# Performance work log

Measured on AMD Instinct MI355X. Metric: run time of the kernel, lower is better.

## Reference

```python
import jax, jax.numpy as jnp
import numpy as np

K = 1024
D = 256
BETA = 0.25


def setup_inputs() -> dict:
    key = jax.random.key(0)
    kx, kc = jax.random.split(key)
    x = jax.random.normal(kx, (64, 32, 32, D), dtype=jnp.float32)
    limit = 1.0 / K
    codebook = jax.random.uniform(kc, (K, D), dtype=jnp.float32, minval=-limit, maxval=limit)
    return {"x": x, "codebook": codebook}


def reference(x, codebook):
    flat = x.reshape(-1, D)                                   # [N, D]
    x2 = jnp.sum(jnp.square(flat), axis=1, keepdims=True)     # [N, 1]
    e2 = jnp.sum(jnp.square(codebook), axis=1)                # [K]
    sim = flat @ codebook.T                                   # [N, K]
    dist = x2 + e2 - 2.0 * sim                                # [N, K]
    idx = jnp.argmin(dist, axis=1)                            # [N]
    q = codebook[idx].reshape(x.shape)                        # [..., D]

    q_st = jax.lax.stop_gradient(q)
    x_st = jax.lax.stop_gradient(x)
    commit = jnp.mean(jnp.square(q_st - x))
    codebk = jnp.mean(jnp.square(q - x_st))
    loss = BETA * commit + codebk

    # code-usage statistics via histogram (equivalent to mean of one-hot)
    counts = jnp.zeros((K,), dtype=x.dtype).at[idx].add(1.0)
    probs = counts / flat.shape[0]
    eps = jnp.asarray(1e-10, dtype=x.dtype)
    H = -jnp.sum(probs * jnp.log2(probs + eps))               # bits/index
    perplexity = jnp.exp(H * jnp.log(jnp.asarray(2.0, dtype=x.dtype)))
    usage = jnp.sum((probs > 0).astype(x.dtype)) / float(K)

    y = x + jax.lax.stop_gradient(q - x)                      # straight-through
    return y, idx, loss, perplexity, usage, H
```

## Files before the change

### kernel.cpp

```cpp
#include <hip/hip_runtime.h>
#include <math.h>

#define D       256
#define KCODES  1024
#define NROWS   65536
#define BETA    0.25f
#define MARGIN  1e-3f
#define MAXSURV 7

typedef __attribute__((ext_vector_type(8))) short bf16x8;
typedef __attribute__((ext_vector_type(4))) float f32x4;

__device__ __forceinline__ unsigned int bf16_rne(float f) {
    unsigned int u = __float_as_uint(f);
    return (u + 0x7FFFu + ((u >> 16) & 1u)) >> 16;
}
__device__ __forceinline__ f32x4 mfma16(bf16x8 a, bf16x8 b, f32x4 c) {
    return __builtin_amdgcn_mfma_f32_16x16x32_bf16(a, b, c, 0, 0, 0);
}

__global__ __launch_bounds__(256) void split_cb_kernel(const float* __restrict__ cb,
                                                       ushort* __restrict__ cs,
                                                       float* __restrict__ e2f) {
    int code = blockIdx.x * 4 + (threadIdx.x >> 6);
    int lane = threadIdx.x & 63;
    float4 v = ((const float4*)(cb + (size_t)code * D))[lane];
    double s = (double)v.x * v.x + (double)v.y * v.y +
               (double)v.z * v.z + (double)v.w * v.w;
    ushort* ph = cs + (size_t)code * 256 + lane * 4;
    ph[0] = (ushort)bf16_rne(v.x); ph[1] = (ushort)bf16_rne(v.y);
    ph[2] = (ushort)bf16_rne(v.z); ph[3] = (ushort)bf16_rne(v.w);
    #pragma unroll
    for (int off = 32; off > 0; off >>= 1) s += __shfl_down(s, off, 64);
    if (lane == 0) e2f[code] = (float)s;
}

__global__ __launch_bounds__(256, 2) void screen_kernel(
    const float* __restrict__ x, const ushort* __restrict__ cs,
    const float* __restrict__ e2f, float* __restrict__ x2f,
    ushort* __restrict__ rowlist)
{
    __shared__ __attribute__((aligned(16))) ushort Bt[2][32 * 264];
    __shared__ float  mrg_d[128][33];
    __shared__ ushort mrg_k[128][33];

    const int tid  = threadIdx.x;
    const int wave = tid >> 6, lane = tid & 63;
    const int quad = lane >> 4, m = lane & 15;
    const int rowBase = blockIdx.x * 128;
    const int wrb = rowBase + wave * 32;

    const int sc = tid & 31, sp = tid >> 5;
    bf16x8 stg[4];
    {
        const ushort* src = cs + (size_t)sc * 256 + sp * 32;
        #pragma unroll
        for (int i = 0; i < 4; ++i) stg[i] = *(const bf16x8*)&src[i * 8];
    }

    bf16x8 af[2][8];
    #pragma unroll
    for (int t = 0; t < 2; ++t) {
        const float* xr = x + (size_t)(wrb + t * 16 + m) * D;
        double s = 0.0;
        #pragma unroll
        for (int c = 0; c < 8; ++c) {
            float4 f0 = *(const float4*)&xr[c * 32 + quad * 8];
            float4 f1 = *(const float4*)&xr[c * 32 + quad * 8 + 4];
            s += (double)f0.x * f0.x + (double)f0.y * f0.y +
                 (double)f0.z * f0.z + (double)f0.w * f0.w;
            s += (double)f1.x * f1.x + (double)f1.y * f1.y +
                 (double)f1.z * f1.z + (double)f1.w * f1.w;
            float ff[8] = {f0.x, f0.y, f0.z, f0.w, f1.x, f1.y, f1.z, f1.w};
            #pragma unroll
            for (int j = 0; j < 8; ++j) af[t][c][j] = (short)bf16_rne(ff[j]);
        }
        s += __shfl_xor(s, 16, 64);
        s += __shfl_xor(s, 32, 64);
        if (quad == 0) x2f[wrb + t * 16 + m] = (float)s;
    }

    float    d1[2][4], d2[2][4];
    unsigned k1[2][4], k2[2][4];
    #pragma unroll
    for (int t = 0; t < 2; ++t)
        #pragma unroll
        for (int r = 0; r < 4; ++r) { d1[t][r] = 1e30f; d2[t][r] = 1e30f; k1[t][r] = 0; k2[t][r] = 0; }

    for (int kt = 0; kt < KCODES / 32; ++kt) {
        {
            ushort* dst = &Bt[kt & 1][sc * 264 + sp * 32];
            #pragma unroll
            for (int i = 0; i < 4; ++i) *(bf16x8*)&dst[i * 8] = stg[i];
        }
        __syncthreads();
        if (kt < KCODES / 32 - 1) {
            const ushort* src = cs + (size_t)((kt + 1) * 32 + sc) * 256 + sp * 32;
            #pragma unroll
            for (int i = 0; i < 4; ++i) stg[i] = *(const bf16x8*)&src[i * 8];
        }

        const ushort* Bcur = &Bt[kt & 1][0];
        #pragma unroll
        for (int nt = 0; nt < 2; ++nt) {
            f32x4 acc0 = {0.f, 0.f, 0.f, 0.f};
            f32x4 acc1 = {0.f, 0.f, 0.f, 0.f};
            const ushort* bp = Bcur + (nt * 16 + m) * 264 + quad * 8;
            __builtin_amdgcn_s_setprio(1);
            #pragma unroll
            for (int c = 0; c < 8; ++c) {
                bf16x8 bh = *(const bf16x8*)&bp[c * 32];
                acc0 = mfma16(af[0][c], bh, acc0);
                acc1 = mfma16(af[1][c], bh, acc1);
            }
            __builtin_amdgcn_s_setprio(0);
            unsigned kcode = kt * 32 + nt * 16 + m;
            float e2 = e2f[kcode];
            #pragma unroll
            for (int t = 0; t < 2; ++t) {
                f32x4 acc = t ? acc1 : acc0;
                #pragma unroll
                for (int r = 0; r < 4; ++r) {
                    float d = fmaf(-2.f, acc[r], e2);
                    bool lt2 = d < d2[t][r];
                    bool lt1 = d < d1[t][r];
                    d2[t][r] = lt2 ? (lt1 ? d1[t][r] : d) : d2[t][r];
                    k2[t][r] = lt2 ? (lt1 ? k1[t][r] : kcode) : k2[t][r];
                    d1[t][r] = lt1 ? d : d1[t][r];
                    k1[t][r] = lt1 ? kcode : k1[t][r];
                }
            }
        }
    }

    #pragma unroll
    for (int t = 0; t < 2; ++t)
        #pragma unroll
        for (int r = 0; r < 4; ++r) {
            int rowloc = wave * 32 + t * 16 + quad * 4 + r;
            mrg_d[rowloc][m * 2 + 0] = d1[t][r];
            mrg_k[rowloc][m * 2 + 0] = (ushort)k1[t][r];
            mrg_d[rowloc][m * 2 + 1] = d2[t][r];
            mrg_k[rowloc][m * 2 + 1] = (ushort)k2[t][r];
        }
    __syncthreads();
    if (tid < 128) {
        float dmin = 1e30f;
        #pragma unroll
        for (int j = 0; j < 32; ++j) dmin = fminf(dmin, mrg_d[tid][j]);
        float lim = dmin + MARGIN;
        ushort out[8] = {0, 0, 0, 0, 0, 0, 0, 0};
        int cnt = 0;
        for (int j = 0; j < 32; ++j) {
            if (mrg_d[tid][j] <= lim && cnt < MAXSURV) { out[1 + cnt] = mrg_k[tid][j]; ++cnt; }
        }
        out[0] = (ushort)cnt;
        *(bf16x8*)&rowlist[(size_t)(rowBase + tid) * 8] = *(bf16x8*)out;
    }
}

__global__ __launch_bounds__(256) void rescore_kernel(
    const float* __restrict__ x, const float* __restrict__ cb,
    const float* __restrict__ x2f, const float* __restrict__ e2f,
    const ushort* __restrict__ rowlist, float* __restrict__ out_idxf,
    unsigned int* __restrict__ counts, float* __restrict__ y,
    float* __restrict__ msepart)
{
    int row  = blockIdx.x * 4 + (threadIdx.x >> 6);
    int lane = threadIdx.x & 63;
    const ushort* lst = rowlist + (size_t)row * 8;
    int cnt = lst[0];
    float4 xv = ((const float4*)(x + (size_t)row * D))[lane];

    int bk;
    if (cnt == 1) {
        bk = lst[1];
    } else {
        float x2 = x2f[row];
        float bestd = 1e30f;
        int   bestk = 0;
        for (int s = 0; s < cnt; ++s) {
            int k = lst[1 + s];
            float4 cv = ((const float4*)(cb + (size_t)k * D))[lane];
            double p = (double)xv.x * cv.x + (double)xv.y * cv.y +
                       (double)xv.z * cv.z + (double)xv.w * cv.w;
            #pragma unroll
            for (int off = 32; off > 0; off >>= 1) p += __shfl_down(p, off, 64);
            float simf = (float)p;
            float tt   = x2 + e2f[k];
            float dq   = tt - 2.0f * simf;
            if (dq < bestd || (dq == bestd && k < bestk)) { bestd = dq; bestk = k; }
        }
        bk = __shfl(bestk, 0, 64);
    }
    if (lane == 0) {
        out_idxf[row] = (float)bk;
        atomicAdd(&counts[bk], 1u);
    }
    float4 q = ((const float4*)(cb + (size_t)bk * D))[lane];
    float4 dv;
    dv.x = q.x - xv.x; dv.y = q.y - xv.y; dv.z = q.z - xv.z; dv.w = q.w - xv.w;
    float4 yv;
    yv.x = xv.x + dv.x; yv.y = xv.y + dv.y; yv.z = xv.z + dv.z; yv.w = xv.w + dv.w;
    ((float4*)(y + (size_t)row * D))[lane] = yv;
    float s = dv.x * dv.x + dv.y * dv.y + dv.z * dv.z + dv.w * dv.w;
    #pragma unroll
    for (int off = 32; off > 0; off >>= 1) s += __shfl_down(s, off, 64);
    if (lane == 0) msepart[row] = s;
}

__global__ __launch_bounds__(1024) void stats_kernel(
    const unsigned int* __restrict__ counts, const float* __restrict__ msepart,
    float* __restrict__ outs)
{
    int t = threadIdx.x;
    float ms = 0.f;
    #pragma unroll
    for (int j = 0; j < 64; ++j) ms += msepart[t + 1024 * j];

    float p = (float)counts[t] * (1.0f / 65536.0f);
    float h = -p * log2f(p + 1e-10f);
    float u = (p > 0.f) ? 1.f : 0.f;
    #pragma unroll
    for (int off = 32; off > 0; off >>= 1) {
        h  += __shfl_down(h,  off, 64);
        u  += __shfl_down(u,  off, 64);
        ms += __shfl_down(ms, off, 64);
    }
    __shared__ float hs[16], us[16], mss[16];
    int lane = t & 63, w = t >> 6;
    if (lane == 0) { hs[w] = h; us[w] = u; mss[w] = ms; }
    __syncthreads();
    if (t == 0) {
        float H = 0.f, U = 0.f, M = 0.f;
        #pragma unroll
        for (int i = 0; i < 16; ++i) { H += hs[i]; U += us[i]; M += mss[i]; }
        float m = M * (1.0f / 16777216.0f);
        float loss = BETA * m + m;
        float perp = expf(H * 0.69314718055994530942f);
        outs[0] = loss;
        outs[1] = perp;
        outs[2] = U * (1.0f / 1024.0f);
        outs[3] = H;
    }
}

extern "C" void kernel_launch(void* const* d_in, const int* in_sizes, int n_in,
                              void* d_out, int out_size, void* d_ws, size_t ws_size,
                              hipStream_t stream) {
    const float* x  = (const float*)d_in[0];
    const float* cb = (const float*)d_in[1];
    float* out      = (float*)d_out;

    float* y        = out;
    float* out_idxf = out + 16777216;
    float* outs     = out + 16777216 + 65536;

    float*        x2f     = (float*)d_ws;
    float*        e2f     = (float*)((char*)d_ws + 262144);
    unsigned int* counts  = (unsigned int*)((char*)d_ws + 266240);
    ushort*       rowlist = (ushort*)((char*)d_ws + 270400);
    ushort*       cs      = (ushort*)((char*)d_ws + 1318976);
    float*        msepart = (float*)((char*)d_ws + 1843264);

    hipMemsetAsync((char*)d_ws + 266240, 0, 4096, stream);
    split_cb_kernel<<<KCODES / 4, 256, 0, stream>>>(cb, cs, e2f);
    screen_kernel<<<NROWS / 128, 256, 0, stream>>>(x, cs, e2f, x2f, rowlist);
    rescore_kernel<<<NROWS / 4, 256, 0, stream>>>(x, cb, x2f, e2f, rowlist,
                                                  out_idxf, counts, y, msepart);
    stats_kernel<<<1, 1024, 0, stream>>>(counts, msepart, outs);
}
```

Measured before the change: 204.4 us.

## Halve screen block size, alias merge buffers onto LDS tile, stagger block starts

The screen kernel now runs 2-wave blocks of 64 rows instead of 4-wave blocks of 128 rows. Each thread stages twice as much codebook data per tile. The merge scratch arrays are aliased onto the idle half of the double-buffered codebook LDS, which cuts LDS per block so more blocks can be resident. Blocks are staggered with s_sleep by blockIdx, and the e2 loads are hoisted to once per tile. The trade-off is that each codebook tile is now reused across half as many rows, so total codebook reads from L2 double.

Measured after the change: 218.4 us. 6.9% more time.

```diff
diff --git a/kernel.cpp b/kernel.cpp
--- a/kernel.cpp
+++ b/kernel.cpp
@@ -35,27 +35,36 @@
     if (lane == 0) e2f[code] = (float)s;
 }
 
-__global__ __launch_bounds__(256, 2) void screen_kernel(
+__global__ __launch_bounds__(128, 2) void screen_kernel(
     const float* __restrict__ x, const ushort* __restrict__ cs,
     const float* __restrict__ e2f, float* __restrict__ x2f,
     ushort* __restrict__ rowlist)
 {
     __shared__ __attribute__((aligned(16))) ushort Bt[2][32 * 264];
-    __shared__ float  mrg_d[128][33];
-    __shared__ ushort mrg_k[128][33];
+    float*  mrg_d = (float*)&Bt[0][0];
+    ushort* mrg_k = (ushort*)((char*)&Bt[0][0] + 64 * 33 * 4);
+    #define MRG_D(r, j) mrg_d[(r) * 33 + (j)]
+    #define MRG_K(r, j) mrg_k[(r) * 33 + (j)]
 
     const int tid  = threadIdx.x;
     const int wave = tid >> 6, lane = tid & 63;
     const int quad = lane >> 4, m = lane & 15;
-    const int rowBase = blockIdx.x * 128;
+    const int rowBase = blockIdx.x * 64;
     const int wrb = rowBase + wave * 32;
 
+    switch (blockIdx.x & 3) {
+        case 1: __builtin_amdgcn_s_sleep(16); break;
+        case 2: __builtin_amdgcn_s_sleep(32); break;
+        case 3: __builtin_amdgcn_s_sleep(48); break;
+        default: break;
+    }
+
     const int sc = tid & 31, sp = tid >> 5;
-    bf16x8 stg[4];
+    bf16x8 stg[8];
     {
-        const ushort* src = cs + (size_t)sc * 256 + sp * 32;
-        #pragma unroll
-        for (int i = 0; i < 4; ++i) stg[i] = *(const bf16x8*)&src[i * 8];
+        const ushort* src = cs + (size_t)sc * 256 + sp * 64;
+        #pragma unroll
+        for (int i = 0; i < 8; ++i) stg[i] = *(const bf16x8*)&src[i * 8];
     }
 
     bf16x8 af[2][8];
@@ -89,16 +98,19 @@
 
     for (int kt = 0; kt < KCODES / 32; ++kt) {
         {
-            ushort* dst = &Bt[kt & 1][sc * 264 + sp * 32];
-            #pragma unroll
-            for (int i = 0; i < 4; ++i) *(bf16x8*)&dst[i * 8] = stg[i];
+            ushort* dst = &Bt[kt & 1][sc * 264 + sp * 64];
+            #pragma unroll
+            for (int i = 0; i < 8; ++i) *(bf16x8*)&dst[i * 8] = stg[i];
         }
         __syncthreads();
         if (kt < KCODES / 32 - 1) {
-            const ushort* src = cs + (size_t)((kt + 1) * 32 + sc) * 256 + sp * 32;
-            #pragma unroll
-            for (int i = 0; i < 4; ++i) stg[i] = *(const bf16x8*)&src[i * 8];
-        }
+            const ushort* src = cs + (size_t)((kt + 1) * 32 + sc) * 256 + sp * 64;
+            #pragma unroll
+            for (int i = 0; i < 8; ++i) stg[i] = *(const bf16x8*)&src[i * 8];
+        }
+
+        float e2a = e2f[kt * 32 + m];
+        float e2b = e2f[kt * 32 + 16 + m];
 
         const ushort* Bcur = &Bt[kt & 1][0];
         #pragma unroll
@@ -115,7 +127,7 @@
             }
             __builtin_amdgcn_s_setprio(0);
             unsigned kcode = kt * 32 + nt * 16 + m;
-            float e2 = e2f[kcode];
+            float e2 = nt ? e2b : e2a;
             #pragma unroll
             for (int t = 0; t < 2; ++t) {
                 f32x4 acc = t ? acc1 : acc0;
@@ -138,25 +150,27 @@
         #pragma unroll
         for (int r = 0; r < 4; ++r) {
             int rowloc = wave * 32 + t * 16 + quad * 4 + r;
-            mrg_d[rowloc][m * 2 + 0] = d1[t][r];
-            mrg_k[rowloc][m * 2 + 0] = (ushort)k1[t][r];
-            mrg_d[rowloc][m * 2 + 1] = d2[t][r];
-            mrg_k[rowloc][m * 2 + 1] = (ushort)k2[t][r];
+            MRG_D(rowloc, m * 2 + 0) = d1[t][r];
+            MRG_K(rowloc, m * 2 + 0) = (ushort)k1[t][r];
+            MRG_D(rowloc, m * 2 + 1) = d2[t][r];
+            MRG_K(rowloc, m * 2 + 1) = (ushort)k2[t][r];
         }
     __syncthreads();
-    if (tid < 128) {
+    if (tid < 64) {
         float dmin = 1e30f;
         #pragma unroll
-        for (int j = 0; j < 32; ++j) dmin = fminf(dmin, mrg_d[tid][j]);
+        for (int j = 0; j < 32; ++j) dmin = fminf(dmin, MRG_D(tid, j));
         float lim = dmin + MARGIN;
         ushort out[8] = {0, 0, 0, 0, 0, 0, 0, 0};
         int cnt = 0;
         for (int j = 0; j < 32; ++j) {
-            if (mrg_d[tid][j] <= lim && cnt < MAXSURV) { out[1 + cnt] = mrg_k[tid][j]; ++cnt; }
+            if (MRG_D(tid, j) <= lim && cnt < MAXSURV) { out[1 + cnt] = MRG_K(tid, j); ++cnt; }
         }
         out[0] = (ushort)cnt;
         *(bf16x8*)&rowlist[(size_t)(rowBase + tid) * 8] = *(bf16x8*)out;
     }
+    #undef MRG_D
+    #undef MRG_K
 }
 
 __global__ __launch_bounds__(256) void rescore_kernel(
@@ -265,7 +279,7 @@
 
     hipMemsetAsync((char*)d_ws + 266240, 0, 4096, stream);
     split_cb_kernel<<<KCODES / 4, 256, 0, stream>>>(cb, cs, e2f);
-    screen_kernel<<<NROWS / 128, 256, 0, stream>>>(x, cs, e2f, x2f, rowlist);
+    screen_kernel<<<NROWS / 64, 128, 0, stream>>>(x, cs, e2f, x2f, rowlist);
     rescore_kernel<<<NROWS / 4, 256, 0, stream>>>(x, cb, x2f, e2f, rowlist,
                                                   out_idxf, counts, y, msepart);
     stats_kernel<<<1, 1024, 0, stream>>>(counts, msepart, outs);
```

## Widen screen tiles to 64 rows per wave and pack distance+index into one key

Applied to the files above, without the earlier changes.

Each wave in the screening GEMM now handles 64 rows instead of 32, so every codebook fragment read from LDS feeds four MFMAs instead of two. Grid size is halved and launch bounds drop to one block per SIMD to make room for the larger register tile. The top-2 tracking packs a truncated, offset-positive float distance with the 10-bit code index into one unsigned key, replacing separate distance/index registers with integer compares. The merge buffer reuses the codebook LDS tile in two phases instead of having its own shared arrays. The risks are lower occupancy, extra register pressure, and the coarser distance precision shifting which candidates fall inside the rescore margin.

New measurement: 221.5 us. +8.4%, slower.

```diff
diff --git a/kernel.cpp b/kernel.cpp
--- a/kernel.cpp
+++ b/kernel.cpp
@@ -35,20 +35,20 @@
     if (lane == 0) e2f[code] = (float)s;
 }
 
-__global__ __launch_bounds__(256, 2) void screen_kernel(
+__global__ __launch_bounds__(256, 1) void screen_kernel(
     const float* __restrict__ x, const ushort* __restrict__ cs,
     const float* __restrict__ e2f, float* __restrict__ x2f,
     ushort* __restrict__ rowlist)
 {
     __shared__ __attribute__((aligned(16))) ushort Bt[2][32 * 264];
-    __shared__ float  mrg_d[128][33];
-    __shared__ ushort mrg_k[128][33];
+    unsigned* mrg = (unsigned*)&Bt[0][0];
+    #define MRG(r, j) mrg[(r) * 33 + (j)]
 
     const int tid  = threadIdx.x;
     const int wave = tid >> 6, lane = tid & 63;
     const int quad = lane >> 4, m = lane & 15;
-    const int rowBase = blockIdx.x * 128;
-    const int wrb = rowBase + wave * 32;
+    const int rowBase = blockIdx.x * 256;
+    const int wrb = rowBase + wave * 64;
 
     const int sc = tid & 31, sp = tid >> 5;
     bf16x8 stg[4];
@@ -58,9 +58,9 @@
         for (int i = 0; i < 4; ++i) stg[i] = *(const bf16x8*)&src[i * 8];
     }
 
-    bf16x8 af[2][8];
-    #pragma unroll
-    for (int t = 0; t < 2; ++t) {
+    bf16x8 af[4][8];
+    #pragma unroll
+    for (int t = 0; t < 4; ++t) {
         const float* xr = x + (size_t)(wrb + t * 16 + m) * D;
         double s = 0.0;
         #pragma unroll
@@ -80,12 +80,11 @@
         if (quad == 0) x2f[wrb + t * 16 + m] = (float)s;
     }
 
-    float    d1[2][4], d2[2][4];
-    unsigned k1[2][4], k2[2][4];
-    #pragma unroll
-    for (int t = 0; t < 2; ++t)
-        #pragma unroll
-        for (int r = 0; r < 4; ++r) { d1[t][r] = 1e30f; d2[t][r] = 1e30f; k1[t][r] = 0; k2[t][r] = 0; }
+    unsigned u1[4][4], u2[4][4];
+    #pragma unroll
+    for (int t = 0; t < 4; ++t)
+        #pragma unroll
+        for (int r = 0; r < 4; ++r) { u1[t][r] = 0xFFFFFFFFu; u2[t][r] = 0xFFFFFFFFu; }
 
     for (int kt = 0; kt < KCODES / 32; ++kt) {
         {
@@ -100,11 +99,16 @@
             for (int i = 0; i < 4; ++i) stg[i] = *(const bf16x8*)&src[i * 8];
         }
 
+        float e2pa = e2f[kt * 32 + m] + 0.5f;
+        float e2pb = e2f[kt * 32 + 16 + m] + 0.5f;
+
         const ushort* Bcur = &Bt[kt & 1][0];
         #pragma unroll
         for (int nt = 0; nt < 2; ++nt) {
             f32x4 acc0 = {0.f, 0.f, 0.f, 0.f};
             f32x4 acc1 = {0.f, 0.f, 0.f, 0.f};
+            f32x4 acc2 = {0.f, 0.f, 0.f, 0.f};
+            f32x4 acc3 = {0.f, 0.f, 0.f, 0.f};
             const ushort* bp = Bcur + (nt * 16 + m) * 264 + quad * 8;
             __builtin_amdgcn_s_setprio(1);
             #pragma unroll
@@ -112,51 +116,59 @@
                 bf16x8 bh = *(const bf16x8*)&bp[c * 32];
                 acc0 = mfma16(af[0][c], bh, acc0);
                 acc1 = mfma16(af[1][c], bh, acc1);
+                acc2 = mfma16(af[2][c], bh, acc2);
+                acc3 = mfma16(af[3][c], bh, acc3);
             }
             __builtin_amdgcn_s_setprio(0);
             unsigned kcode = kt * 32 + nt * 16 + m;
-            float e2 = e2f[kcode];
-            #pragma unroll
-            for (int t = 0; t < 2; ++t) {
-                f32x4 acc = t ? acc1 : acc0;
+            float e2p = nt ? e2pb : e2pa;
+            #pragma unroll
+            for (int t = 0; t < 4; ++t) {
+                f32x4 acc = (t == 0) ? acc0 : (t == 1) ? acc1 : (t == 2) ? acc2 : acc3;
                 #pragma unroll
                 for (int r = 0; r < 4; ++r) {
-                    float d = fmaf(-2.f, acc[r], e2);
-                    bool lt2 = d < d2[t][r];
-                    bool lt1 = d < d1[t][r];
-                    d2[t][r] = lt2 ? (lt1 ? d1[t][r] : d) : d2[t][r];
-                    k2[t][r] = lt2 ? (lt1 ? k1[t][r] : kcode) : k2[t][r];
-                    d1[t][r] = lt1 ? d : d1[t][r];
-                    k1[t][r] = lt1 ? kcode : k1[t][r];
+                    float d = fmaf(-2.f, acc[r], e2p);
+                    unsigned u = (__float_as_uint(d) & 0xFFFFFC00u) | kcode;
+                    bool lt1 = u < u1[t][r];
+                    bool lt2 = u < u2[t][r];
+                    u2[t][r] = lt2 ? (lt1 ? u1[t][r] : u) : u2[t][r];
+                    u1[t][r] = lt1 ? u : u1[t][r];
                 }
             }
         }
     }
 
     #pragma unroll
-    for (int t = 0; t < 2; ++t)
-        #pragma unroll
-        for (int r = 0; r < 4; ++r) {
-            int rowloc = wave * 32 + t * 16 + quad * 4 + r;
-            mrg_d[rowloc][m * 2 + 0] = d1[t][r];
-            mrg_k[rowloc][m * 2 + 0] = (ushort)k1[t][r];
-            mrg_d[rowloc][m * 2 + 1] = d2[t][r];
-            mrg_k[rowloc][m * 2 + 1] = (ushort)k2[t][r];
-        }
-    __syncthreads();
-    if (tid < 128) {
-        float dmin = 1e30f;
-        #pragma unroll
-        for (int j = 0; j < 32; ++j) dmin = fminf(dmin, mrg_d[tid][j]);
-        float lim = dmin + MARGIN;
-        ushort out[8] = {0, 0, 0, 0, 0, 0, 0, 0};
-        int cnt = 0;
-        for (int j = 0; j < 32; ++j) {
-            if (mrg_d[tid][j] <= lim && cnt < MAXSURV) { out[1 + cnt] = mrg_k[tid][j]; ++cnt; }
-        }
-        out[0] = (ushort)cnt;
-        *(bf16x8*)&rowlist[(size_t)(rowBase + tid) * 8] = *(bf16x8*)out;
-    }
+    for (int ph = 0; ph < 2; ++ph) {
+        if ((wave >> 1) == ph) {
+            #pragma unroll
+            for (int t = 0; t < 4; ++t)
+                #pragma unroll
+                for (int r = 0; r < 4; ++r) {
+                    int rowloc = (wave & 1) * 64 + t * 16 + quad * 4 + r;
+                    MRG(rowloc, m * 2 + 0) = u1[t][r];
+                    MRG(rowloc, m * 2 + 1) = u2[t][r];
+                }
+        }
+        __syncthreads();
+        if (tid < 128) {
+            unsigned umin = 0xFFFFFFFFu;
+            #pragma unroll
+            for (int j = 0; j < 32; ++j) umin = min(umin, MRG(tid, j));
+            float dfloor = __uint_as_float(umin & 0xFFFFFC00u);
+            unsigned limu = (__float_as_uint(dfloor + MARGIN) & 0xFFFFFC00u) | 1023u;
+            ushort out[8] = {0, 0, 0, 0, 0, 0, 0, 0};
+            int cnt = 0;
+            for (int j = 0; j < 32; ++j) {
+                unsigned u = MRG(tid, j);
+                if (u <= limu && cnt < MAXSURV) { out[1 + cnt] = (ushort)(u & 1023u); ++cnt; }
+            }
+            out[0] = (ushort)cnt;
+            *(bf16x8*)&rowlist[(size_t)(rowBase + ph * 128 + tid) * 8] = *(bf16x8*)out;
+        }
+        __syncthreads();
+    }
+    #undef MRG
 }
 
 __global__ __launch_bounds__(256) void rescore_kernel(
@@ -265,7 +277,7 @@
 
     hipMemsetAsync((char*)d_ws + 266240, 0, 4096, stream);
     split_cb_kernel<<<KCODES / 4, 256, 0, stream>>>(cb, cs, e2f);
-    screen_kernel<<<NROWS / 128, 256, 0, stream>>>(x, cs, e2f, x2f, rowlist);
+    screen_kernel<<<NROWS / 256, 256, 0, stream>>>(x, cs, e2f, x2f, rowlist);
     rescore_kernel<<<NROWS / 4, 256, 0, stream>>>(x, cb, x2f, e2f, rowlist,
                                                   out_idxf, counts, y, msepart);
     stats_kernel<<<1, 1024, 0, stream>>>(counts, msepart, outs);
```
